# Optimization experiments

Hardware: AMD Instinct MI355X
Metric: run time of the kernel (lower is better)

## Reference

```python
import jax, jax.numpy as jnp
import numpy as np

N_EMBD = 768
N_HEAD = 12
HEAD_DIM = N_EMBD // N_HEAD
HIDDEN = 4 * N_EMBD
B, T = 4, 2048
EPS = 1e-5


def setup_inputs() -> dict:
    key = jax.random.key(0)
    ks = jax.random.split(key, 7)
    s = lambda fan_in: 1.0 / np.sqrt(fan_in)
    return {
        "x": jax.random.normal(ks[0], (B, T, N_EMBD), dtype=jnp.float32),
        "ln1_g": jnp.ones((N_EMBD,), jnp.float32),
        "ln1_b": jnp.zeros((N_EMBD,), jnp.float32),
        "W_attn": jax.random.normal(ks[1], (N_EMBD, 3 * N_EMBD), jnp.float32) * s(N_EMBD),
        "W_o": jax.random.normal(ks[2], (N_EMBD, N_EMBD), jnp.float32) * s(N_EMBD),
        "ln2_g": jnp.ones((N_EMBD,), jnp.float32),
        "ln2_b": jnp.zeros((N_EMBD,), jnp.float32),
        "W_fc": jax.random.normal(ks[3], (N_EMBD, HIDDEN), jnp.float32) * s(N_EMBD),
        "W_proj": jax.random.normal(ks[4], (HIDDEN, N_EMBD), jnp.float32) * s(HIDDEN),
    }


def _layernorm(x, g, b):
    mu = jnp.mean(x, axis=-1, keepdims=True)
    var = jnp.mean(jnp.square(x - mu), axis=-1, keepdims=True)
    return (x - mu) * jax.lax.rsqrt(var + EPS) * g + b


def _attention(x, W_attn, W_o):
    b, t, c = x.shape
    qkv = x @ W_attn  # [B,T,3C]
    q, k, v = jnp.split(qkv, 3, axis=-1)
    # [B,H,T,D]
    q = q.reshape(b, t, N_HEAD, HEAD_DIM).transpose(0, 2, 1, 3)
    k = k.reshape(b, t, N_HEAD, HEAD_DIM).transpose(0, 2, 1, 3)
    v = v.reshape(b, t, N_HEAD, HEAD_DIM).transpose(0, 2, 1, 3)
    scale = 1.0 / jnp.sqrt(jnp.float32(HEAD_DIM))
    att = jnp.einsum("bhqd,bhkd->bhqk", q, k) * scale  # [B,H,T,T]
    causal = jnp.arange(t)[:, None] >= jnp.arange(t)[None, :]
    att = jnp.where(causal, att, -jnp.inf)
    att = jax.nn.softmax(att, axis=-1)
    y = jnp.einsum("bhqk,bhkd->bhqd", att, v)
    y = y.transpose(0, 2, 1, 3).reshape(b, t, c)
    return y @ W_o


def reference(x, ln1_g, ln1_b, W_attn, W_o, ln2_g, ln2_b, W_fc, W_proj):
    x = x + _attention(_layernorm(x, ln1_g, ln1_b), W_attn, W_o)
    h = _layernorm(x, ln2_g, ln2_b)
    h = jax.nn.gelu(h @ W_fc, approximate=False) @ W_proj  # torch nn.GELU() is exact erf gelu
    return x + h
```

## Files before the change

kernel.cpp:

```cpp
#include <hip/hip_runtime.h>
#include <cstdint>
#include <cstddef>

#define B_ 4
#define T_ 2048
#define C_ 768
#define H_ 12
#define D_ 64
#define M_ (B_*T_)
#define C3_ 2304
#define HID_ 3072

typedef unsigned short ushort_t;
typedef __bf16 bf16x8_t __attribute__((ext_vector_type(8)));
typedef float f32x4 __attribute__((ext_vector_type(4)));

typedef const __attribute__((address_space(1))) void* gas_ptr;
typedef __attribute__((address_space(3))) void* las_ptr;

__device__ __forceinline__ void gload_lds16(const ushort_t* g, ushort_t* l) {
  __builtin_amdgcn_global_load_lds((gas_ptr)g, (las_ptr)l, 16, 0, 0);
}

__device__ __forceinline__ float bf2f(ushort_t h) {
  union { unsigned int u; float f; } cv; cv.u = ((unsigned int)h) << 16; return cv.f;
}
__device__ __forceinline__ ushort_t f2bf(float f) {
  union { float f; unsigned int u; } cv; cv.f = f;
  unsigned int u = cv.u;
  unsigned int r = (u + 0x7FFFu + ((u >> 16) & 1u)) >> 16;
  return (ushort_t)r;
}
__device__ __forceinline__ ushort_t f2bf_trunc(float f) {
  union { float f; unsigned int u; } cv; cv.f = f;
  return (ushort_t)(cv.u >> 16);
}

__global__ __launch_bounds__(256) void transpose_k(const float* __restrict__ in,
                                                   ushort_t* __restrict__ out, int K, int N) {
  __shared__ ushort_t tile[32][33];
  int nx = threadIdx.x, ky = threadIdx.y;
  int n0 = blockIdx.x * 32, k0 = blockIdx.y * 32;
#pragma unroll
  for (int i = 0; i < 4; i++)
    tile[ky + i * 8][nx] = f2bf(in[(size_t)(k0 + ky + i * 8) * N + n0 + nx]);
  __syncthreads();
#pragma unroll
  for (int i = 0; i < 4; i++)
    out[(size_t)(n0 + ky + i * 8) * K + k0 + nx] = tile[nx][ky + i * 8];
}

__global__ __launch_bounds__(256) void vtrans_k(const ushort_t* __restrict__ qkv,
                                                ushort_t* __restrict__ vg) {
  __shared__ ushort_t tile[32][33];
  int nx = threadIdx.x, ky = threadIdx.y;
  int t0 = blockIdx.x * 32, d0 = blockIdx.y * 32;
  int bh = blockIdx.z;
  int b = bh / H_, h = bh % H_;
  const ushort_t* src = qkv + (size_t)b * T_ * C3_ + 2 * C_ + h * D_;
#pragma unroll
  for (int i = 0; i < 4; i++)
    tile[ky + i * 8][nx] = src[(size_t)(t0 + ky + i * 8) * C3_ + d0 + nx];
  __syncthreads();
  ushort_t* dst = vg + (size_t)bh * D_ * T_;
#pragma unroll
  for (int i = 0; i < 4; i++)
    dst[(size_t)(d0 + ky + i * 8) * T_ + t0 + nx] = tile[nx][ky + i * 8];
}

__global__ __launch_bounds__(256) void ln_k(const float* __restrict__ x, const float* __restrict__ g,
                                            const float* __restrict__ bb, ushort_t* __restrict__ out) {
  __shared__ float red[8];
  int row = blockIdx.x, t = threadIdx.x;
  const float* xr = x + (size_t)row * C_;
  float v0 = xr[t], v1 = xr[t + 256], v2 = xr[t + 512];
  float s = v0 + v1 + v2;
  float s2 = v0 * v0 + v1 * v1 + v2 * v2;
#pragma unroll
  for (int m = 32; m >= 1; m >>= 1) { s += __shfl_xor(s, m); s2 += __shfl_xor(s2, m); }
  int w = t >> 6;
  if ((t & 63) == 0) { red[w * 2] = s; red[w * 2 + 1] = s2; }
  __syncthreads();
  s = red[0] + red[2] + red[4] + red[6];
  s2 = red[1] + red[3] + red[5] + red[7];
  float mu = s * (1.f / C_);
  float var = s2 * (1.f / C_) - mu * mu;
  float rstd = rsqrtf(var + 1e-5f);
  out[(size_t)row * C_ + t]       = f2bf((v0 - mu) * rstd * g[t] + bb[t]);
  out[(size_t)row * C_ + t + 256] = f2bf((v1 - mu) * rstd * g[t + 256] + bb[t + 256]);
  out[(size_t)row * C_ + t + 512] = f2bf((v2 - mu) * rstd * g[t + 512] + bb[t + 512]);
}

#define MFMA16(d, a, b) d = __builtin_amdgcn_mfma_f32_16x16x32_bf16(a, b, d, 0, 0, 0)

template <int EPI>
__global__ void gemm_bt_k(const ushort_t* __restrict__ A,
                          const ushort_t* __restrict__ Bt,
                          const float* __restrict__ res,
                          void* __restrict__ outp,
                          int N, int K) {
  __shared__ __align__(16) ushort_t As[128][32];
  __shared__ __align__(16) ushort_t Bs[128][32];
  int t = threadIdx.x;
  int bn = blockIdx.x * 128, bm = blockIdx.y * 128;
  int lane = t & 63, w = t >> 6;
  int wm = (w >> 1) * 64, wn = (w & 1) * 64;
  int lm = lane & 15, q8 = (lane >> 4) * 8;

  int lr = lane >> 2, lc = (lane & 3) * 8;
  const ushort_t* ga0 = A  + (size_t)(bm + w * 16 + lr) * K + lc;
  const ushort_t* gb0 = Bt + (size_t)(bn + w * 16 + lr) * K + lc;
  const size_t kstep64 = (size_t)64 * K;
  ushort_t* la0 = &As[w * 16][0];
  ushort_t* la1 = &As[w * 16 + 64][0];
  ushort_t* lb0 = &Bs[w * 16][0];
  ushort_t* lb1 = &Bs[w * 16 + 64][0];

  const f32x4 fz = {0.f, 0.f, 0.f, 0.f};
  f32x4 acc00 = fz, acc01 = fz, acc02 = fz, acc03 = fz;
  f32x4 acc10 = fz, acc11 = fz, acc12 = fz, acc13 = fz;
  f32x4 acc20 = fz, acc21 = fz, acc22 = fz, acc23 = fz;
  f32x4 acc30 = fz, acc31 = fz, acc32 = fz, acc33 = fz;

  for (int k0 = 0; k0 < K; k0 += 32) {
    __syncthreads();
    gload_lds16(ga0 + k0, la0);
    gload_lds16(ga0 + kstep64 + k0, la1);
    gload_lds16(gb0 + k0, lb0);
    gload_lds16(gb0 + kstep64 + k0, lb1);
    __syncthreads();
    bf16x8_t af0 = *(const bf16x8_t*)&As[wm + lm][q8];
    bf16x8_t af1 = *(const bf16x8_t*)&As[wm + 16 + lm][q8];
    bf16x8_t af2 = *(const bf16x8_t*)&As[wm + 32 + lm][q8];
    bf16x8_t af3 = *(const bf16x8_t*)&As[wm + 48 + lm][q8];
    bf16x8_t bg0 = *(const bf16x8_t*)&Bs[wn + lm][q8];
    bf16x8_t bg1 = *(const bf16x8_t*)&Bs[wn + 16 + lm][q8];
    bf16x8_t bg2 = *(const bf16x8_t*)&Bs[wn + 32 + lm][q8];
    bf16x8_t bg3 = *(const bf16x8_t*)&Bs[wn + 48 + lm][q8];
    MFMA16(acc00, af0, bg0); MFMA16(acc01, af0, bg1); MFMA16(acc02, af0, bg2); MFMA16(acc03, af0, bg3);
    MFMA16(acc10, af1, bg0); MFMA16(acc11, af1, bg1); MFMA16(acc12, af1, bg2); MFMA16(acc13, af1, bg3);
    MFMA16(acc20, af2, bg0); MFMA16(acc21, af2, bg1); MFMA16(acc22, af2, bg2); MFMA16(acc23, af2, bg3);
    MFMA16(acc30, af3, bg0); MFMA16(acc31, af3, bg1); MFMA16(acc32, af3, bg2); MFMA16(acc33, af3, bg3);
  }

  int rowb = bm + wm + (lane >> 4) * 4;
  int colb = bn + wn + lm;

#define ST(vv, row, jj) do { \
    float v = (vv); \
    size_t idx = (size_t)(row) * N + colb + (jj) * 16; \
    if constexpr (EPI == 0) { ((ushort_t*)outp)[idx] = f2bf(v); } \
    else if constexpr (EPI == 1) { ((float*)outp)[idx] = v + res[idx]; } \
    else { float gl = 0.5f * v * (1.0f + erff(v * 0.70710678118654752f)); \
           ((ushort_t*)outp)[idx] = f2bf(gl); } \
  } while (0)
#define STROW(a0, a1, a2, a3, row, rr) \
    ST(a0[rr], row, 0); ST(a1[rr], row, 1); ST(a2[rr], row, 2); ST(a3[rr], row, 3);
#define STBLK(a0, a1, a2, a3, rbase) \
    STROW(a0, a1, a2, a3, (rbase), 0) STROW(a0, a1, a2, a3, (rbase) + 1, 1) \
    STROW(a0, a1, a2, a3, (rbase) + 2, 2) STROW(a0, a1, a2, a3, (rbase) + 3, 3)

  STBLK(acc00, acc01, acc02, acc03, rowb)
  STBLK(acc10, acc11, acc12, acc13, rowb + 16)
  STBLK(acc20, acc21, acc22, acc23, rowb + 32)
  STBLK(acc30, acc31, acc32, acc33, rowb + 48)
#undef ST
#undef STROW
#undef STBLK
}

__device__ __forceinline__ void stage64(const ushort_t* __restrict__ g, size_t strideE,
                                        ushort_t* l, int w, int lane) {
  int rl = lane >> 3;
  int ce = ((lane & 7) ^ rl) << 3;
  const ushort_t* g0 = g + (size_t)(w * 16 + rl) * strideE + ce;
  gload_lds16(g0, l + (size_t)(w * 16) * 64);
  const ushort_t* g1 = g + (size_t)(w * 16 + 8 + rl) * strideE + ce;
  gload_lds16(g1, l + (size_t)(w * 16 + 8) * 64);
}

__global__ __launch_bounds__(256, 3) void attn_k(const ushort_t* __restrict__ qkv,
                                                 const ushort_t* __restrict__ vg,
                                                 ushort_t* __restrict__ y) {
  __shared__ __align__(16) ushort_t Ks[2][64][64];
  __shared__ __align__(16) ushort_t Vs[2][64][64];
  __shared__ __align__(16) ushort_t Ps[4][16][72];

  int t = threadIdx.x;
  int w = t >> 6, lane = t & 63;
  int lm = lane & 15, qq = lane >> 4, q8 = qq * 8;
  int bh = blockIdx.x;
  int qt = (int)gridDim.y - 1 - (int)blockIdx.y;
  int b = bh / H_, h = bh % H_;

  size_t baserow = (size_t)b * T_;
  const ushort_t* qkvb = qkv + baserow * C3_ + h * D_;
  const ushort_t* kbase = qkvb + C_;
  const ushort_t* vbase = vg + (size_t)bh * D_ * T_;

  int qrow0 = qt * 64 + w * 16;
  const ushort_t* qp = qkvb + (size_t)(qrow0 + lm) * C3_ + q8;
  bf16x8_t aq0 = *(const bf16x8_t*)(qp);
  bf16x8_t aq1 = *(const bf16x8_t*)(qp + 32);
  __builtin_amdgcn_s_waitcnt(0);

  const f32x4 fz = {0.f, 0.f, 0.f, 0.f};
  f32x4 aO0 = fz, aO1 = fz, aO2 = fz, aO3 = fz;
  f32x4 lsum = fz;

  const float SC = 0.125f * 1.44269504088896340736f;

#define BODY(CUR, KT, MASKED)                                                   \
  {                                                                             \
    const char* Kb = (const char*)&Ks[CUR][0][0];                               \
    const char* Vb = (const char*)&Vs[CUR][0][0];                               \
    const int rsw = (lm & 7) << 4;                                              \
    const int c0 = (qq * 16) ^ rsw;                                             \
    const int c1 = (64 + qq * 16) ^ rsw;                                        \
    bf16x8_t kf[8], vv[8];                                                      \
    _Pragma("unroll") for (int j = 0; j < 4; j++) {                             \
      int rb = (j * 16 + lm) << 7;                                              \
      kf[2*j]   = *(const bf16x8_t*)(Kb + rb + c0);                             \
      kf[2*j+1] = *(const bf16x8_t*)(Kb + rb + c1);                             \
      vv[2*j]   = *(const bf16x8_t*)(Vb + rb + c0);                             \
      vv[2*j+1] = *(const bf16x8_t*)(Vb + rb + c1);                             \
    }                                                                           \
    f32x4 sa0 = fz, sa1 = fz, sa2 = fz, sa3 = fz;                               \
    MFMA16(sa0, aq0, kf[0]); MFMA16(sa0, aq1, kf[1]);                           \
    MFMA16(sa1, aq0, kf[2]); MFMA16(sa1, aq1, kf[3]);                           \
    MFMA16(sa2, aq0, kf[4]); MFMA16(sa2, aq1, kf[5]);                           \
    MFMA16(sa3, aq0, kf[6]); MFMA16(sa3, aq1, kf[7]);                           \
    _Pragma("unroll") for (int j = 0; j < 4; j++) {                             \
      f32x4 sj = (j == 0) ? sa0 : (j == 1) ? sa1 : (j == 2) ? sa2 : sa3;        \
      _Pragma("unroll") for (int r2 = 0; r2 < 4; r2++) {                        \
        float v = sj[r2] * SC;                                                  \
        if (MASKED && (j * 16 + lm) > (w * 16 + qq * 4 + r2)) v = -1e30f;       \
        float p = exp2f(v);                                                     \
        lsum[r2] += p;                                                          \
        Ps[w][qq * 4 + r2][j * 16 + lm] = f2bf_trunc(p);                        \
      }                                                                         \
    }                                                                           \
    {                                                                           \
      bf16x8_t ap_lo = *(const bf16x8_t*)&Ps[w][lm][q8];                        \
      bf16x8_t ap_hi = *(const bf16x8_t*)&Ps[w][lm][32 + q8];                   \
      MFMA16(aO0, ap_lo, vv[0]); MFMA16(aO0, ap_hi, vv[1]);                     \
      MFMA16(aO1, ap_lo, vv[2]); MFMA16(aO1, ap_hi, vv[3]);                     \
      MFMA16(aO2, ap_lo, vv[4]); MFMA16(aO2, ap_hi, vv[5]);                     \
      MFMA16(aO3, ap_lo, vv[6]); MFMA16(aO3, ap_hi, vv[7]);                     \
    }                                                                           \
  }

  stage64(kbase, C3_, &Ks[0][0][0], w, lane);
  stage64(vbase, T_, &Vs[0][0][0], w, lane);
  int cur = 0;
  for (int kt = 0; kt <= qt; ++kt) {
    if (kt < qt) {
      stage64(kbase + (size_t)(kt + 1) * 64 * C3_, C3_, &Ks[cur ^ 1][0][0], w, lane);
      stage64(vbase + (size_t)(kt + 1) * 64,       T_,  &Vs[cur ^ 1][0][0], w, lane);
      asm volatile("s_waitcnt vmcnt(4)" ::: "memory");
    } else {
      asm volatile("s_waitcnt vmcnt(0)" ::: "memory");
    }
    __builtin_amdgcn_s_barrier();
    asm volatile("" ::: "memory");
    if (kt == qt) { BODY(cur, kt, true) }
    else          { BODY(cur, kt, false) }
    asm volatile("" ::: "memory");
    __builtin_amdgcn_s_barrier();
    cur ^= 1;
  }
#undef BODY

#pragma unroll
  for (int r2 = 0; r2 < 4; r2++) {
    float s = lsum[r2];
    s += __shfl_xor(s, 1);
    s += __shfl_xor(s, 2);
    s += __shfl_xor(s, 4);
    s += __shfl_xor(s, 8);
    float inv = 1.f / s;
    size_t orow = (baserow + qrow0 + qq * 4 + r2) * C_ + h * D_;
    y[orow + lm]      = f2bf(aO0[r2] * inv);
    y[orow + 16 + lm] = f2bf(aO1[r2] * inv);
    y[orow + 32 + lm] = f2bf(aO2[r2] * inv);
    y[orow + 48 + lm] = f2bf(aO3[r2] * inv);
  }
}

extern "C" void kernel_launch(void* const* d_in, const int* in_sizes, int n_in,
                              void* d_out, int out_size, void* d_ws, size_t ws_size,
                              hipStream_t stream) {
  (void)in_sizes; (void)n_in; (void)out_size; (void)ws_size;
  const float* x      = (const float*)d_in[0];
  const float* ln1_g  = (const float*)d_in[1];
  const float* ln1_b  = (const float*)d_in[2];
  const float* W_attn = (const float*)d_in[3];
  const float* W_o    = (const float*)d_in[4];
  const float* ln2_g  = (const float*)d_in[5];
  const float* ln2_b  = (const float*)d_in[6];
  const float* W_fc   = (const float*)d_in[7];
  const float* W_proj = (const float*)d_in[8];

  char* ws = (char*)d_ws;
  ushort_t* big  = (ushort_t*)(ws);
  ushort_t* Vg   = (ushort_t*)(ws + 37748736);
  ushort_t* tmp  = (ushort_t*)(ws + 50331648);
  float*    x2   = (float*)   (ws + 62914560);
  ushort_t* Wat  = (ushort_t*)(ws + 88080384);
  ushort_t* Wot  = (ushort_t*)(ws + 91619328);
  ushort_t* Wfct = (ushort_t*)(ws + 92798976);
  ushort_t* Wpt  = (ushort_t*)(ws + 97517568);

  dim3 tb(32, 8);
  transpose_k<<<dim3(C3_ / 32, C_ / 32), tb, 0, stream>>>(W_attn, Wat, C_, C3_);
  transpose_k<<<dim3(C_ / 32, C_ / 32), tb, 0, stream>>>(W_o, Wot, C_, C_);
  transpose_k<<<dim3(HID_ / 32, C_ / 32), tb, 0, stream>>>(W_fc, Wfct, C_, HID_);
  transpose_k<<<dim3(C_ / 32, HID_ / 32), tb, 0, stream>>>(W_proj, Wpt, HID_, C_);

  ln_k<<<M_, 256, 0, stream>>>(x, ln1_g, ln1_b, tmp);
  gemm_bt_k<0><<<dim3(C3_ / 128, M_ / 128), 256, 0, stream>>>(tmp, Wat, nullptr, big, C3_, C_);
  vtrans_k<<<dim3(T_ / 32, D_ / 32, B_ * H_), tb, 0, stream>>>(big, Vg);
  attn_k<<<dim3(B_ * H_, T_ / 64), 256, 0, stream>>>(big, Vg, tmp);
  gemm_bt_k<1><<<dim3(C_ / 128, M_ / 128), 256, 0, stream>>>(tmp, Wot, x, x2, C_, C_);
  ln_k<<<M_, 256, 0, stream>>>(x2, ln2_g, ln2_b, tmp);
  gemm_bt_k<2><<<dim3(HID_ / 128, M_ / 128), 256, 0, stream>>>(tmp, Wfct, nullptr, big, HID_, C_);
  gemm_bt_k<1><<<dim3(C_ / 128, M_ / 128), 256, 0, stream>>>(big, Wpt, x2, d_out, C_, HID_);
}
```

Before: 401.6 us.

## Double-buffer GEMM LDS tiles and swizzle workgroup order for L2 reuse

The GEMM main loop now uses two LDS buffers, so the global-to-LDS load for the next K-slice is issued before computing the current one. Synchronisation uses explicit vmcnt waits and raw barriers in place of __syncthreads. A workgroup index remap groups blocks into strided sets to improve L2 locality. This doubles LDS use per block, which may reduce occupancy, and relies on manual waitcnt counts being correct.

```diff
diff --git a/kernel.cpp b/kernel.cpp
--- a/kernel.cpp
+++ b/kernel.cpp
@@ -99,10 +99,16 @@
                           const float* __restrict__ res,
                           void* __restrict__ outp,
                           int N, int K) {
-  __shared__ __align__(16) ushort_t As[128][32];
-  __shared__ __align__(16) ushort_t Bs[128][32];
+  __shared__ __align__(16) ushort_t As[2][128][32];
+  __shared__ __align__(16) ushort_t Bs[2][128][32];
   int t = threadIdx.x;
-  int bn = blockIdx.x * 128, bm = blockIdx.y * 128;
+
+  int nwg = (int)(gridDim.x * gridDim.y);
+  int orig = (int)(blockIdx.y * gridDim.x + blockIdx.x);
+  int swz = (nwg & 7) ? orig : ((orig & 7) * (nwg >> 3) + (orig >> 3));
+  int bx = swz % (int)gridDim.x, by = swz / (int)gridDim.x;
+  int bn = bx * 128, bm = by * 128;
+
   int lane = t & 63, w = t >> 6;
   int wm = (w >> 1) * 64, wn = (w & 1) * 64;
   int lm = lane & 15, q8 = (lane >> 4) * 8;
@@ -111,10 +117,6 @@
   const ushort_t* ga0 = A  + (size_t)(bm + w * 16 + lr) * K + lc;
   const ushort_t* gb0 = Bt + (size_t)(bn + w * 16 + lr) * K + lc;
   const size_t kstep64 = (size_t)64 * K;
-  ushort_t* la0 = &As[w * 16][0];
-  ushort_t* la1 = &As[w * 16 + 64][0];
-  ushort_t* lb0 = &Bs[w * 16][0];
-  ushort_t* lb1 = &Bs[w * 16 + 64][0];
 
   const f32x4 fz = {0.f, 0.f, 0.f, 0.f};
   f32x4 acc00 = fz, acc01 = fz, acc02 = fz, acc03 = fz;
@@ -122,26 +124,51 @@
   f32x4 acc20 = fz, acc21 = fz, acc22 = fz, acc23 = fz;
   f32x4 acc30 = fz, acc31 = fz, acc32 = fz, acc33 = fz;
 
-  for (int k0 = 0; k0 < K; k0 += 32) {
-    __syncthreads();
-    gload_lds16(ga0 + k0, la0);
-    gload_lds16(ga0 + kstep64 + k0, la1);
-    gload_lds16(gb0 + k0, lb0);
-    gload_lds16(gb0 + kstep64 + k0, lb1);
-    __syncthreads();
-    bf16x8_t af0 = *(const bf16x8_t*)&As[wm + lm][q8];
-    bf16x8_t af1 = *(const bf16x8_t*)&As[wm + 16 + lm][q8];
-    bf16x8_t af2 = *(const bf16x8_t*)&As[wm + 32 + lm][q8];
-    bf16x8_t af3 = *(const bf16x8_t*)&As[wm + 48 + lm][q8];
-    bf16x8_t bg0 = *(const bf16x8_t*)&Bs[wn + lm][q8];
-    bf16x8_t bg1 = *(const bf16x8_t*)&Bs[wn + 16 + lm][q8];
-    bf16x8_t bg2 = *(const bf16x8_t*)&Bs[wn + 32 + lm][q8];
-    bf16x8_t bg3 = *(const bf16x8_t*)&Bs[wn + 48 + lm][q8];
-    MFMA16(acc00, af0, bg0); MFMA16(acc01, af0, bg1); MFMA16(acc02, af0, bg2); MFMA16(acc03, af0, bg3);
-    MFMA16(acc10, af1, bg0); MFMA16(acc11, af1, bg1); MFMA16(acc12, af1, bg2); MFMA16(acc13, af1, bg3);
-    MFMA16(acc20, af2, bg0); MFMA16(acc21, af2, bg1); MFMA16(acc22, af2, bg2); MFMA16(acc23, af2, bg3);
-    MFMA16(acc30, af3, bg0); MFMA16(acc31, af3, bg1); MFMA16(acc32, af3, bg2); MFMA16(acc33, af3, bg3);
+#define STAGE(BUF, KOFF) do {                                   \
+    gload_lds16(ga0 + (KOFF), &As[BUF][w * 16][0]);             \
+    gload_lds16(ga0 + kstep64 + (KOFF), &As[BUF][w * 16 + 64][0]); \
+    gload_lds16(gb0 + (KOFF), &Bs[BUF][w * 16][0]);             \
+    gload_lds16(gb0 + kstep64 + (KOFF), &Bs[BUF][w * 16 + 64][0]); \
+  } while (0)
+
+#define COMPUTE(BUF) do {                                            \
+    bf16x8_t af0 = *(const bf16x8_t*)&As[BUF][wm + lm][q8];          \
+    bf16x8_t af1 = *(const bf16x8_t*)&As[BUF][wm + 16 + lm][q8];     \
+    bf16x8_t af2 = *(const bf16x8_t*)&As[BUF][wm + 32 + lm][q8];     \
+    bf16x8_t af3 = *(const bf16x8_t*)&As[BUF][wm + 48 + lm][q8];     \
+    bf16x8_t bg0 = *(const bf16x8_t*)&Bs[BUF][wn + lm][q8];          \
+    bf16x8_t bg1 = *(const bf16x8_t*)&Bs[BUF][wn + 16 + lm][q8];     \
+    bf16x8_t bg2 = *(const bf16x8_t*)&Bs[BUF][wn + 32 + lm][q8];     \
+    bf16x8_t bg3 = *(const bf16x8_t*)&Bs[BUF][wn + 48 + lm][q8];     \
+    MFMA16(acc00, af0, bg0); MFMA16(acc01, af0, bg1); MFMA16(acc02, af0, bg2); MFMA16(acc03, af0, bg3); \
+    MFMA16(acc10, af1, bg0); MFMA16(acc11, af1, bg1); MFMA16(acc12, af1, bg2); MFMA16(acc13, af1, bg3); \
+    MFMA16(acc20, af2, bg0); MFMA16(acc21, af2, bg1); MFMA16(acc22, af2, bg2); MFMA16(acc23, af2, bg3); \
+    MFMA16(acc30, af3, bg0); MFMA16(acc31, af3, bg1); MFMA16(acc32, af3, bg2); MFMA16(acc33, af3, bg3); \
+  } while (0)
+
+  STAGE(0, 0);
+  for (int k0 = 0; k0 < K; k0 += 64) {
+    STAGE(1, k0 + 32);
+    asm volatile("s_waitcnt vmcnt(4)" ::: "memory");
+    __builtin_amdgcn_s_barrier();
+    asm volatile("" ::: "memory");
+    COMPUTE(0);
+    asm volatile("" ::: "memory");
+    __builtin_amdgcn_s_barrier();
+    if (k0 + 64 < K) {
+      STAGE(0, k0 + 64);
+      asm volatile("s_waitcnt vmcnt(4)" ::: "memory");
+    } else {
+      asm volatile("s_waitcnt vmcnt(0)" ::: "memory");
+    }
+    __builtin_amdgcn_s_barrier();
+    asm volatile("" ::: "memory");
+    COMPUTE(1);
+    asm volatile("" ::: "memory");
+    __builtin_amdgcn_s_barrier();
   }
+#undef STAGE
+#undef COMPUTE
 
   int rowb = bm + wm + (lane >> 4) * 4;
   int colb = bn + wn + lm;
```

New measurement: 380.3 us. 1.06x faster.
